# Performance work log

Hardware: AMD Instinct MI355X
Metric: run time of the kernel (lower is better)

## Reference

```python
import jax, jax.numpy as jnp
import numpy as np


def _fake_quant(x, num_bits):
    # Per-tensor uniform min/max fake quantization with STE (straight-through).
    qmax = float(2 ** num_bits - 1)
    mn = jnp.min(x)
    mx = jnp.max(x)
    scale = (mx - mn) / qmax
    q = jnp.round((x - mn) / scale) * scale + mn
    return x + jax.lax.stop_gradient(q - x)


def _qlinear(x, W, b, num_bits):
    xq = _fake_quant(x, num_bits)
    Wq = _fake_quant(W, num_bits)
    return xq @ Wq.T + b


def setup_inputs() -> dict:
    key = jax.random.key(0)
    ks = jax.random.split(key, 7)
    B, D, H = 8192, 1024, 1024
    s = 1.0 / np.sqrt(H)
    return {
        "input": jax.random.normal(ks[0], (B, D), jnp.float32),
        "h": jax.random.normal(ks[1], (B, H), jnp.float32),
        "c": jax.random.normal(ks[2], (B, H), jnp.float32),
        "W_in": jax.random.normal(ks[3], (4 * H, D), jnp.float32) * s,
        "b_in": jax.random.normal(ks[4], (4 * H,), jnp.float32) * s,
        "W_h": jax.random.normal(ks[5], (4 * H, H), jnp.float32) * s,
        "b_h": jax.random.normal(ks[6], (4 * H,), jnp.float32) * s,
        "num_bits": 8,
        "num_bits_grad": 8,
    }


def reference(input, h, c, W_in, b_in, W_h, b_h, num_bits, num_bits_grad):
    B = input.shape[0]
    Hd = h.shape[1]
    mixed_input = _qlinear(input, W_in, b_in, num_bits).reshape(B, 4, Hd)
    mixed_hidden = _qlinear(h, W_h, b_h, num_bits).reshape(B, 4, Hd)
    gates = mixed_input + mixed_hidden  # [B, 4, H]
    i = jax.nn.sigmoid(gates[:, 0, :])
    f = jax.nn.sigmoid(gates[:, 1, :])
    g = jnp.tanh(gates[:, 2, :])
    o = jax.nn.sigmoid(gates[:, 3, :])
    c_ = f * c + i * g
    h_ = o * jnp.tanh(c_)
    return (h_, c_)
```

## Files before the change

kernel.cpp:

```cpp
#include <hip/hip_runtime.h>
#include <hip/hip_bf16.h>

typedef unsigned short u16;
typedef int i32x4 __attribute__((ext_vector_type(4)));
typedef signed char s8;

#define NB_RED 256

__global__ void k_minmax_partial(const float* __restrict__ x, const float* __restrict__ h,
                                 const float* __restrict__ wi, const float* __restrict__ wh,
                                 float* __restrict__ partials) {
    int t = blockIdx.y;
    const float* p = (t == 0) ? x : (t == 1) ? h : (t == 2) ? wi : wh;
    int n4 = ((t < 2) ? (8192 * 1024) : (4096 * 1024)) >> 2;
    float mn = 3.4e38f, mx = -3.4e38f;
    const float4* p4 = (const float4*)p;
    for (int i = blockIdx.x * blockDim.x + threadIdx.x; i < n4; i += gridDim.x * blockDim.x) {
        float4 v = p4[i];
        mn = fminf(mn, fminf(fminf(v.x, v.y), fminf(v.z, v.w)));
        mx = fmaxf(mx, fmaxf(fmaxf(v.x, v.y), fmaxf(v.z, v.w)));
    }
    for (int d = 1; d < 64; d <<= 1) {
        mn = fminf(mn, __shfl_xor(mn, d));
        mx = fmaxf(mx, __shfl_xor(mx, d));
    }
    __shared__ float smn[4], smx[4];
    int wv = threadIdx.x >> 6;
    if ((threadIdx.x & 63) == 0) { smn[wv] = mn; smx[wv] = mx; }
    __syncthreads();
    if (threadIdx.x == 0) {
        mn = fminf(fminf(smn[0], smn[1]), fminf(smn[2], smn[3]));
        mx = fmaxf(fmaxf(smx[0], smx[1]), fmaxf(smx[2], smx[3]));
        partials[(t * NB_RED + blockIdx.x) * 2 + 0] = mn;
        partials[(t * NB_RED + blockIdx.x) * 2 + 1] = mx;
    }
}

__global__ void k_minmax_final(const float* __restrict__ partials, const int* __restrict__ nbits,
                               float* __restrict__ params) {
    int t = blockIdx.x;
    int tid = threadIdx.x;
    float mn = partials[(t * NB_RED + tid) * 2 + 0];
    float mx = partials[(t * NB_RED + tid) * 2 + 1];
    for (int d = 1; d < 64; d <<= 1) {
        mn = fminf(mn, __shfl_xor(mn, d));
        mx = fmaxf(mx, __shfl_xor(mx, d));
    }
    __shared__ float smn[4], smx[4];
    int wv = tid >> 6;
    if ((tid & 63) == 0) { smn[wv] = mn; smx[wv] = mx; }
    __syncthreads();
    if (tid == 0) {
        mn = fminf(fminf(smn[0], smn[1]), fminf(smn[2], smn[3]));
        mx = fmaxf(fmaxf(smx[0], smx[1]), fmaxf(smx[2], smx[3]));
        float qmax = (float)((1u << (*nbits)) - 1u);
        params[t * 2 + 0] = mn;
        params[t * 2 + 1] = (mx - mn) / qmax;
    }
}

static __device__ __forceinline__ int block_reduce_i(int v, int tid) {
    for (int d = 1; d < 64; d <<= 1) v += __shfl_xor(v, d);
    __shared__ int sred[4];
    if ((tid & 63) == 0) sred[tid >> 6] = v;
    __syncthreads();
    return sred[0] + sred[1] + sred[2] + sred[3];
}

__global__ void k_quant_A(const float* __restrict__ x, const float* __restrict__ h,
                          const float* __restrict__ params, s8* __restrict__ A8,
                          float* __restrict__ Rax, float* __restrict__ Rah) {
    int b = blockIdx.x;
    int tsel = b >> 13;
    int row = b & 8191;
    const float* src = tsel ? h : x;
    float mn = params[tsel * 2 + 0], s = params[tsel * 2 + 1];
    int t = threadIdx.x;
    float4 v = ((const float4*)(src + (size_t)row * 1024))[t];
    int k0 = (int)fminf(255.f, fmaxf(0.f, rintf((v.x - mn) / s)));
    int k1 = (int)fminf(255.f, fmaxf(0.f, rintf((v.y - mn) / s)));
    int k2 = (int)fminf(255.f, fmaxf(0.f, rintf((v.z - mn) / s)));
    int k3 = (int)fminf(255.f, fmaxf(0.f, rintf((v.w - mn) / s)));
    unsigned p = ((unsigned)((k0 - 128) & 0xff)) | ((unsigned)((k1 - 128) & 0xff) << 8) |
                 ((unsigned)((k2 - 128) & 0xff) << 16) | ((unsigned)((k3 - 128) & 0xff) << 24);
    *(unsigned*)(A8 + (size_t)row * 2048 + tsel * 1024 + t * 4) = p;
    int sum = block_reduce_i(k0 + k1 + k2 + k3 - 512, t);
    if (t == 0) (tsel ? Rah : Rax)[row] = (float)sum;
}

__global__ void k_quant_W(const float* __restrict__ wi, const float* __restrict__ wh,
                          const float* __restrict__ params, s8* __restrict__ W8,
                          float* __restrict__ Rbi, float* __restrict__ Rbh) {
    int b = blockIdx.x;
    int tsel = b >> 12;
    int row = b & 4095;
    const float* src = tsel ? wh : wi;
    float mn = params[(2 + tsel) * 2 + 0], s = params[(2 + tsel) * 2 + 1];
    int g = row >> 10, j = row & 1023;
    int prow = (j >> 4) * 64 + g * 16 + (j & 15);
    int t = threadIdx.x;
    float4 v = ((const float4*)(src + (size_t)row * 1024))[t];
    int k0 = (int)fminf(255.f, fmaxf(0.f, rintf((v.x - mn) / s)));
    int k1 = (int)fminf(255.f, fmaxf(0.f, rintf((v.y - mn) / s)));
    int k2 = (int)fminf(255.f, fmaxf(0.f, rintf((v.z - mn) / s)));
    int k3 = (int)fminf(255.f, fmaxf(0.f, rintf((v.w - mn) / s)));
    unsigned p = ((unsigned)((k0 - 128) & 0xff)) | ((unsigned)((k1 - 128) & 0xff) << 8) |
                 ((unsigned)((k2 - 128) & 0xff) << 16) | ((unsigned)((k3 - 128) & 0xff) << 24);
    *(unsigned*)(W8 + (size_t)prow * 2048 + tsel * 1024 + t * 4) = p;
    int sum = block_reduce_i(k0 + k1 + k2 + k3 - 512, t);
    if (t == 0) (tsel ? Rbh : Rbi)[prow] = (float)sum;
}

__global__ void k_bias(const float* __restrict__ b_in, const float* __restrict__ b_h,
                       float* __restrict__ bc) {
    int n = blockIdx.x * 256 + threadIdx.x;
    int j = (n >> 6) * 16 + (n & 15);
    int g = (n >> 4) & 3;
    bc[n] = b_in[g * 1024 + j] + b_h[g * 1024 + j];
}

__global__ __launch_bounds__(256, 2) void k_gemm_lstm(
    const s8* __restrict__ A8, const s8* __restrict__ W8,
    const float* __restrict__ params, const float* __restrict__ bc,
    const float* __restrict__ Rax, const float* __restrict__ Rah,
    const float* __restrict__ Rbi, const float* __restrict__ Rbh,
    const float* __restrict__ c_in, float* __restrict__ out) {
    __shared__ __align__(16) s8 As[128 * 64];
    __shared__ __align__(16) s8 Bs[128 * 64];

    const int tid = threadIdx.x;
    const int wave = tid >> 6, lane = tid & 63;
    const int wr = wave >> 1, wc = wave & 1;
    const int la = lane & 15, hi = lane >> 4;
    const int bm = blockIdx.y * 128, bn = blockIdx.x * 128;

    const int srow = lane >> 2;
    const int skb = (((lane & 3) ^ ((srow >> 1) & 3)) * 16);
    const int fR = (la >> 1) & 3;

    i32x4 acc1[4][4], acc2[4][4];
#pragma unroll
    for (int m = 0; m < 4; m++)
#pragma unroll
        for (int n = 0; n < 4; n++) { acc1[m][n] = (i32x4)0; acc2[m][n] = (i32x4)0; }

#define KSTEP(ACC, K0)                                                                       \
    do {                                                                                     \
        _Pragma("unroll") for (int j2 = 0; j2 < 2; ++j2) {                                   \
            int rg = (j2 * 4 + wave) * 16 + srow;                                            \
            __builtin_amdgcn_global_load_lds(                                                \
                (const __attribute__((address_space(1))) void*)(A8 + (size_t)(bm + rg) * 2048 + (K0) + skb), \
                (__attribute__((address_space(3))) void*)&As[(j2 * 4 + wave) * 1024], 16, 0, 0); \
            __builtin_amdgcn_global_load_lds(                                                \
                (const __attribute__((address_space(1))) void*)(W8 + (size_t)(bn + rg) * 2048 + (K0) + skb), \
                (__attribute__((address_space(3))) void*)&Bs[(j2 * 4 + wave) * 1024], 16, 0, 0); \
        }                                                                                    \
        __syncthreads();                                                                     \
        i32x4 af[4], bfr[4];                                                                 \
        _Pragma("unroll") for (int m = 0; m < 4; m++)                                        \
            af[m] = *(const i32x4*)&As[(wr * 64 + m * 16 + la) * 64 + ((hi ^ fR) * 16)];     \
        _Pragma("unroll") for (int n = 0; n < 4; n++)                                        \
            bfr[n] = *(const i32x4*)&Bs[(wc * 64 + n * 16 + la) * 64 + ((hi ^ fR) * 16)];    \
        _Pragma("unroll") for (int m = 0; m < 4; m++)                                        \
            _Pragma("unroll") for (int n = 0; n < 4; n++)                                    \
                ACC[m][n] = __builtin_amdgcn_mfma_i32_16x16x64_i8(af[m], bfr[n], ACC[m][n], 0, 0, 0); \
        __syncthreads();                                                                     \
    } while (0)

    for (int ks = 0; ks < 16; ++ks) KSTEP(acc1, ks * 64);
    for (int ks = 16; ks < 32; ++ks) KSTEP(acc2, ks * 64);
#undef KSTEP

    float mna = params[0], sa = params[1], mnh = params[2], sh = params[3];
    float mni = params[4], si = params[5], mnw = params[6], sw = params[7];
    float za = mna + 128.0f * sa, zi = mni + 128.0f * si;
    float zh = mnh + 128.0f * sh, zw = mnw + 128.0f * sw;
    float C0 = 1024.0f * (za * zi + zh * zw);
    float cax = sa * zi, cah = sh * zw;
    float cbx = si * za, cbh = sw * zh;
    float csx = sa * si, csh = sh * sw;

    const int nb = bn + wc * 64;
    float colt[4];
#pragma unroll
    for (int g = 0; g < 4; ++g) {
        int np = nb + g * 16 + la;
        colt[g] = bc[np] + cbx * Rbi[np] + cbh * Rbh[np] + C0;
    }
    const int ub = (nb >> 6) * 16 + la;

#pragma unroll
    for (int m = 0; m < 4; m++) {
#pragma unroll
        for (int q = 0; q < 4; q++) {
            int row = bm + wr * 64 + m * 16 + 4 * hi + q;
            float rterm = cax * Rax[row] + cah * Rah[row];
            float g0 = colt[0] + rterm + csx * (float)acc1[m][0][q] + csh * (float)acc2[m][0][q];
            float g1 = colt[1] + rterm + csx * (float)acc1[m][1][q] + csh * (float)acc2[m][1][q];
            float g2 = colt[2] + rterm + csx * (float)acc1[m][2][q] + csh * (float)acc2[m][2][q];
            float g3 = colt[3] + rterm + csx * (float)acc1[m][3][q] + csh * (float)acc2[m][3][q];
            float iv = 1.0f / (1.0f + __expf(-g0));
            float fv = 1.0f / (1.0f + __expf(-g1));
            float gv = tanhf(g2);
            float ov = 1.0f / (1.0f + __expf(-g3));
            size_t off = (size_t)row * 1024 + ub;
            float cv = c_in[off];
            float cn = fv * cv + iv * gv;
            float hn = ov * tanhf(cn);
            out[off] = hn;
            out[(size_t)8192 * 1024 + off] = cn;
        }
    }
}

extern "C" void kernel_launch(void* const* d_in, const int* in_sizes, int n_in,
                              void* d_out, int out_size, void* d_ws, size_t ws_size,
                              hipStream_t stream) {
    const float* x = (const float*)d_in[0];
    const float* h = (const float*)d_in[1];
    const float* c = (const float*)d_in[2];
    const float* wi = (const float*)d_in[3];
    const float* bi = (const float*)d_in[4];
    const float* wh = (const float*)d_in[5];
    const float* bh = (const float*)d_in[6];
    const int* nbits = (const int*)d_in[7];
    float* out = (float*)d_out;

    char* ws = (char*)d_ws;
    float* params   = (float*)ws;
    float* partials = (float*)(ws + 64);
    float* bc  = (float*)(ws + 16384);
    float* Rax = (float*)(ws + 32768);
    float* Rah = (float*)(ws + 65536);
    float* Rbi = (float*)(ws + 98304);
    float* Rbh = (float*)(ws + 114688);
    s8* A8 = (s8*)(ws + 131072);
    s8* W8 = (s8*)(ws + 131072 + (size_t)16 * 1024 * 1024);

    k_minmax_partial<<<dim3(NB_RED, 4), 256, 0, stream>>>(x, h, wi, wh, partials);
    k_minmax_final<<<4, 256, 0, stream>>>(partials, nbits, params);
    k_quant_A<<<16384, 256, 0, stream>>>(x, h, params, A8, Rax, Rah);
    k_quant_W<<<8192, 256, 0, stream>>>(wi, wh, params, W8, Rbi, Rbh);
    k_bias<<<16, 256, 0, stream>>>(bi, bh, bc);
    k_gemm_lstm<<<dim3(32, 64), 256, 0, stream>>>(A8, W8, params, bc, Rax, Rah, Rbi, Rbh, c, out);
}
```

Baseline: 165.3 us.

## Triple-buffer LDS tiles in int8 GEMM with async prefetch two steps ahead

Replaces the single-buffered load/sync/compute/sync loop with a three-stage LDS ring. Global-to-LDS loads for tile T+2 are issued before computing tile T. Each step waits only on the older outstanding loads (vmcnt(4)) and uses one barrier. This is meant to hide global memory latency behind the MFMA work and halve the barrier count. In exchange, LDS use triples per block, which could limit occupancy, and correctness now depends on manual wait counts.

```diff
diff --git a/kernel.cpp b/kernel.cpp
--- a/kernel.cpp
+++ b/kernel.cpp
@@ -125,8 +125,8 @@
     const float* __restrict__ Rax, const float* __restrict__ Rah,
     const float* __restrict__ Rbi, const float* __restrict__ Rbh,
     const float* __restrict__ c_in, float* __restrict__ out) {
-    __shared__ __align__(16) s8 As[128 * 64];
-    __shared__ __align__(16) s8 Bs[128 * 64];
+    __shared__ __align__(16) s8 As[3][128 * 64];
+    __shared__ __align__(16) s8 Bs[3][128 * 64];
 
     const int tid = threadIdx.x;
     const int wave = tid >> 6, lane = tid & 63;
@@ -144,32 +144,63 @@
 #pragma unroll
         for (int n = 0; n < 4; n++) { acc1[m][n] = (i32x4)0; acc2[m][n] = (i32x4)0; }
 
-#define KSTEP(ACC, K0)                                                                       \
-    do {                                                                                     \
-        _Pragma("unroll") for (int j2 = 0; j2 < 2; ++j2) {                                   \
-            int rg = (j2 * 4 + wave) * 16 + srow;                                            \
-            __builtin_amdgcn_global_load_lds(                                                \
-                (const __attribute__((address_space(1))) void*)(A8 + (size_t)(bm + rg) * 2048 + (K0) + skb), \
-                (__attribute__((address_space(3))) void*)&As[(j2 * 4 + wave) * 1024], 16, 0, 0); \
-            __builtin_amdgcn_global_load_lds(                                                \
-                (const __attribute__((address_space(1))) void*)(W8 + (size_t)(bn + rg) * 2048 + (K0) + skb), \
-                (__attribute__((address_space(3))) void*)&Bs[(j2 * 4 + wave) * 1024], 16, 0, 0); \
-        }                                                                                    \
-        __syncthreads();                                                                     \
-        i32x4 af[4], bfr[4];                                                                 \
-        _Pragma("unroll") for (int m = 0; m < 4; m++)                                        \
-            af[m] = *(const i32x4*)&As[(wr * 64 + m * 16 + la) * 64 + ((hi ^ fR) * 16)];     \
-        _Pragma("unroll") for (int n = 0; n < 4; n++)                                        \
-            bfr[n] = *(const i32x4*)&Bs[(wc * 64 + n * 16 + la) * 64 + ((hi ^ fR) * 16)];    \
-        _Pragma("unroll") for (int m = 0; m < 4; m++)                                        \
-            _Pragma("unroll") for (int n = 0; n < 4; n++)                                    \
-                ACC[m][n] = __builtin_amdgcn_mfma_i32_16x16x64_i8(af[m], bfr[n], ACC[m][n], 0, 0, 0); \
-        __syncthreads();                                                                     \
+#define STAGE(B, T)                                                                               \
+    do {                                                                                          \
+        _Pragma("unroll") for (int j2 = 0; j2 < 2; ++j2) {                                        \
+            int rg = (j2 * 4 + wave) * 16 + srow;                                                 \
+            __builtin_amdgcn_global_load_lds(                                                     \
+                (const __attribute__((address_space(1))) void*)(A8 + (size_t)(bm + rg) * 2048 + (T) * 64 + skb), \
+                (__attribute__((address_space(3))) void*)&As[(B)][(j2 * 4 + wave) * 1024], 16, 0, 0); \
+            __builtin_amdgcn_global_load_lds(                                                     \
+                (const __attribute__((address_space(1))) void*)(W8 + (size_t)(bn + rg) * 2048 + (T) * 64 + skb), \
+                (__attribute__((address_space(3))) void*)&Bs[(B)][(j2 * 4 + wave) * 1024], 16, 0, 0); \
+        }                                                                                         \
     } while (0)
 
-    for (int ks = 0; ks < 16; ++ks) KSTEP(acc1, ks * 64);
-    for (int ks = 16; ks < 32; ++ks) KSTEP(acc2, ks * 64);
-#undef KSTEP
+#define COMPUTE(B, ACC)                                                                           \
+    do {                                                                                          \
+        i32x4 af[4], bf[4];                                                                       \
+        _Pragma("unroll") for (int m = 0; m < 4; m++)                                             \
+            af[m] = *(const i32x4*)&As[(B)][(wr * 64 + m * 16 + la) * 64 + ((hi ^ fR) * 16)];     \
+        _Pragma("unroll") for (int n = 0; n < 4; n++)                                             \
+            bf[n] = *(const i32x4*)&Bs[(B)][(wc * 64 + n * 16 + la) * 64 + ((hi ^ fR) * 16)];     \
+        _Pragma("unroll") for (int m = 0; m < 4; m++)                                             \
+            _Pragma("unroll") for (int n = 0; n < 4; n++)                                         \
+                ACC[m][n] = __builtin_amdgcn_mfma_i32_16x16x64_i8(af[m], bf[n], ACC[m][n], 0, 0, 0); \
+    } while (0)
+
+#define VMCNT4 asm volatile("s_waitcnt vmcnt(4)" ::: "memory")
+#define VMCNT0 asm volatile("s_waitcnt vmcnt(0)" ::: "memory")
+#define BAR __builtin_amdgcn_s_barrier()
+
+#define STEP(B, T)                                                                                \
+    do {                                                                                          \
+        STAGE(((B) + 2) % 3, (T) + 2);                                                            \
+        if ((T) < 16) COMPUTE(B, acc1); else COMPUTE(B, acc2);                                    \
+        VMCNT4; BAR;                                                                              \
+    } while (0)
+
+    STAGE(0, 0);
+    STAGE(1, 1);
+    VMCNT4; BAR;
+
+#pragma unroll 1
+    for (int i = 0; i < 10; ++i) {
+        int t0 = 3 * i;
+        STEP(0, t0 + 0);
+        STEP(1, t0 + 1);
+        STEP(2, t0 + 2);
+    }
+    COMPUTE(0, acc2);
+    VMCNT0; BAR;
+    COMPUTE(1, acc2);
+
+#undef STEP
+#undef VMCNT4
+#undef VMCNT0
+#undef BAR
+#undef STAGE
+#undef COMPUTE
 
     float mna = params[0], sa = params[1], mnh = params[2], sh = params[3];
     float mni = params[4], si = params[5], mnw = params[6], sw = params[7];
```

New measurement: 174.4 us. +5.5%, slower.

## Load GEMM fragments directly to registers with triple-buffered prefetch and swizzled block order

Applied to the files above, without the earlier changes.

The int8 GEMM kernel drops LDS staging and the two barriers per k-step. Each wave now loads its MFMA operand fragments straight from global memory into registers, using a three-stage register ring that prefetches two k-tiles ahead, and raises wave priority around the MFMA bursts. The launch grid becomes 1D with a remapped block order meant to improve L2 reuse across neighbouring blocks. Without LDS sharing, each wave fetches its own A and B rows, so global and L2 traffic rises. The triple buffers also add substantial register pressure under launch_bounds(256,2).

```diff
diff --git a/kernel.cpp b/kernel.cpp
--- a/kernel.cpp
+++ b/kernel.cpp
@@ -125,18 +125,25 @@
     const float* __restrict__ Rax, const float* __restrict__ Rah,
     const float* __restrict__ Rbi, const float* __restrict__ Rbh,
     const float* __restrict__ c_in, float* __restrict__ out) {
-    __shared__ __align__(16) s8 As[128 * 64];
-    __shared__ __align__(16) s8 Bs[128 * 64];
-
     const int tid = threadIdx.x;
     const int wave = tid >> 6, lane = tid & 63;
     const int wr = wave >> 1, wc = wave & 1;
     const int la = lane & 15, hi = lane >> 4;
-    const int bm = blockIdx.y * 128, bn = blockIdx.x * 128;
-
-    const int srow = lane >> 2;
-    const int skb = (((lane & 3) ^ ((srow >> 1) & 3)) * 16);
-    const int fR = (la >> 1) & 3;
+
+    const int bid = blockIdx.x;
+    const int l = bid >> 3;
+    const int bx = l >> 3;
+    const int by = (bid & 7) * 8 + (l & 7);
+    const int bm = by * 128, bn = bx * 128;
+
+    const s8* aP[4];
+    const s8* bP[4];
+#pragma unroll
+    for (int m = 0; m < 4; ++m)
+        aP[m] = A8 + (size_t)(bm + wr * 64 + m * 16 + la) * 2048 + hi * 16;
+#pragma unroll
+    for (int n = 0; n < 4; ++n)
+        bP[n] = W8 + (size_t)(bn + wc * 64 + n * 16 + la) * 2048 + hi * 16;
 
     i32x4 acc1[4][4], acc2[4][4];
 #pragma unroll
@@ -144,32 +151,36 @@
 #pragma unroll
         for (int n = 0; n < 4; n++) { acc1[m][n] = (i32x4)0; acc2[m][n] = (i32x4)0; }
 
-#define KSTEP(ACC, K0)                                                                       \
-    do {                                                                                     \
-        _Pragma("unroll") for (int j2 = 0; j2 < 2; ++j2) {                                   \
-            int rg = (j2 * 4 + wave) * 16 + srow;                                            \
-            __builtin_amdgcn_global_load_lds(                                                \
-                (const __attribute__((address_space(1))) void*)(A8 + (size_t)(bm + rg) * 2048 + (K0) + skb), \
-                (__attribute__((address_space(3))) void*)&As[(j2 * 4 + wave) * 1024], 16, 0, 0); \
-            __builtin_amdgcn_global_load_lds(                                                \
-                (const __attribute__((address_space(1))) void*)(W8 + (size_t)(bn + rg) * 2048 + (K0) + skb), \
-                (__attribute__((address_space(3))) void*)&Bs[(j2 * 4 + wave) * 1024], 16, 0, 0); \
-        }                                                                                    \
-        __syncthreads();                                                                     \
-        i32x4 af[4], bfr[4];                                                                 \
-        _Pragma("unroll") for (int m = 0; m < 4; m++)                                        \
-            af[m] = *(const i32x4*)&As[(wr * 64 + m * 16 + la) * 64 + ((hi ^ fR) * 16)];     \
-        _Pragma("unroll") for (int n = 0; n < 4; n++)                                        \
-            bfr[n] = *(const i32x4*)&Bs[(wc * 64 + n * 16 + la) * 64 + ((hi ^ fR) * 16)];    \
-        _Pragma("unroll") for (int m = 0; m < 4; m++)                                        \
-            _Pragma("unroll") for (int n = 0; n < 4; n++)                                    \
-                ACC[m][n] = __builtin_amdgcn_mfma_i32_16x16x64_i8(af[m], bfr[n], ACC[m][n], 0, 0, 0); \
-        __syncthreads();                                                                     \
+    i32x4 ast[3][4], bst[3][4];
+
+#define LOADT(S, T)                                                     \
+    do {                                                                \
+        _Pragma("unroll") for (int m = 0; m < 4; ++m)                   \
+            ast[S][m] = *(const i32x4*)(aP[m] + (T) * 64);              \
+        _Pragma("unroll") for (int n = 0; n < 4; ++n)                   \
+            bst[S][n] = *(const i32x4*)(bP[n] + (T) * 64);              \
     } while (0)
 
-    for (int ks = 0; ks < 16; ++ks) KSTEP(acc1, ks * 64);
-    for (int ks = 16; ks < 32; ++ks) KSTEP(acc2, ks * 64);
-#undef KSTEP
+#define COMPUTET(S, ACC)                                                \
+    do {                                                                \
+        _Pragma("unroll") for (int m = 0; m < 4; ++m)                   \
+            _Pragma("unroll") for (int n = 0; n < 4; ++n)               \
+                ACC[m][n] = __builtin_amdgcn_mfma_i32_16x16x64_i8(      \
+                    ast[S][m], bst[S][n], ACC[m][n], 0, 0, 0);          \
+    } while (0)
+
+    LOADT(0, 0);
+    LOADT(1, 1);
+#pragma unroll
+    for (int t = 0; t < 32; ++t) {
+        if (t + 2 < 32) LOADT((t + 2) % 3, t + 2);
+        __builtin_amdgcn_s_setprio(1);
+        if (t < 16) COMPUTET(t % 3, acc1); else COMPUTET(t % 3, acc2);
+        __builtin_amdgcn_s_setprio(0);
+    }
+
+#undef LOADT
+#undef COMPUTET
 
     float mna = params[0], sa = params[1], mnh = params[2], sh = params[3];
     float mni = params[4], si = params[5], mnw = params[6], sw = params[7];
@@ -242,5 +253,5 @@
     k_quant_A<<<16384, 256, 0, stream>>>(x, h, params, A8, Rax, Rah);
     k_quant_W<<<8192, 256, 0, stream>>>(wi, wh, params, W8, Rbi, Rbh);
     k_bias<<<16, 256, 0, stream>>>(bi, bh, bc);
-    k_gemm_lstm<<<dim3(32, 64), 256, 0, stream>>>(A8, W8, params, bc, Rax, Rah, Rbi, Rbh, c, out);
-}
+    k_gemm_lstm<<<2048, 256, 0, stream>>>(A8, W8, params, bc, Rax, Rah, Rbi, Rbh, c, out);
+}
```

After: 291.6 us. 76.4% more time.
